# Performance work log

Measured on AMD Instinct MI355X. Metric: run time of the kernel, lower is better.

## Reference

```python
import jax, jax.numpy as jnp
import numpy as np

N_NODES = 50000
IN_CH, HID, OUT_CH = 512, 128, 64
N_EDGES = 800000


def gcn_conv(x, edge_index, W, b, num_nodes):
    # PyG GCNConv: add self-loops, symmetric deg^{-1/2} normalization,
    # linear transform then scatter-add aggregation at target nodes.
    row, col = edge_index[0], edge_index[1]
    loop = jnp.arange(num_nodes, dtype=row.dtype)
    rows = jnp.concatenate([row, loop])  # sources
    cols = jnp.concatenate([col, loop])  # targets
    deg = jax.ops.segment_sum(jnp.ones_like(cols, dtype=x.dtype), cols, num_segments=num_nodes)
    dinv = jnp.where(deg > 0, jax.lax.rsqrt(deg), 0.0)
    norm = dinv[rows] * dinv[cols]  # [E+N]
    h = x @ W  # [N, out]
    msg = norm[:, None] * h[rows]  # gather + scale
    out = jax.ops.segment_sum(msg, cols, num_segments=num_nodes)
    return out + b


def setup_inputs() -> dict:
    key = jax.random.key(0)
    k = jax.random.split(key, 8)
    x = jax.random.normal(k[0], (N_NODES, IN_CH), dtype=jnp.float32)
    pos_edge_index = jax.random.randint(k[1], (2, N_EDGES), 0, N_NODES, dtype=jnp.int64 if jax.config.jax_enable_x64 else jnp.int32)
    neg_edge_index = jax.random.randint(k[2], (2, N_EDGES), 0, N_NODES, dtype=pos_edge_index.dtype)
    # Glorot-ish init for weights, zeros for bias (PyG default)
    W1 = jax.random.normal(k[3], (IN_CH, HID), dtype=jnp.float32) * (1.0 / np.sqrt(IN_CH))
    b1 = jnp.zeros((HID,), dtype=jnp.float32)
    W2 = jax.random.normal(k[4], (HID, OUT_CH), dtype=jnp.float32) * (1.0 / np.sqrt(HID))
    b2 = jnp.zeros((OUT_CH,), dtype=jnp.float32)
    return {"x": x, "pos_edge_index": pos_edge_index, "neg_edge_index": neg_edge_index,
            "W1": W1, "b1": b1, "W2": W2, "b2": b2}


def reference(x, pos_edge_index, neg_edge_index, W1, b1, W2, b2):
    n = x.shape[0]
    h = gcn_conv(x, pos_edge_index, W1, b1, n)
    h = jax.nn.relu(h)
    z = gcn_conv(h, pos_edge_index, W2, b2, n)  # encode
    edge_index = jnp.concatenate([pos_edge_index, neg_edge_index], axis=-1)
    # decode: per-edge dot product of endpoint embeddings
    logits = jnp.sum(z[edge_index[0]] * z[edge_index[1]], axis=-1)
    return logits
```

## Files before the change

kernel.cpp:

```cpp
#include <hip/hip_runtime.h>

#define WAVE 64
#define CAP 64

typedef __bf16 v8bf __attribute__((ext_vector_type(8)));
typedef __bf16 v4bf __attribute__((ext_vector_type(4)));
typedef __bf16 v2bf __attribute__((ext_vector_type(2)));
typedef float f32x4 __attribute__((ext_vector_type(4)));

__device__ __forceinline__ void async16(void* lds, const void* g) {
    __builtin_amdgcn_global_load_lds((const __attribute__((address_space(1))) void*)g,
                                     (__attribute__((address_space(3))) void*)lds, 16, 0, 0);
}

__global__ __launch_bounds__(256) void prep_kernel(const float* __restrict__ W1,
                                                   const float* __restrict__ W2,
                                                   __bf16* __restrict__ Wt1hi,
                                                   __bf16* __restrict__ Wt1lo,
                                                   __bf16* __restrict__ Wt2hi,
                                                   __bf16* __restrict__ Wt2lo) {
    int b = blockIdx.x;
    int tid = threadIdx.x;
    if (b < 256) {
        int idx = b * 256 + tid;
        int k = idx >> 7, n = idx & 127;
        float v = W1[idx];
        __bf16 h = (__bf16)v;
        Wt1hi[n * 512 + k] = h;
        Wt1lo[n * 512 + k] = (__bf16)(v - (float)h);
    } else {
        int idx = (b - 256) * 256 + tid;
        int k = idx >> 6, n = idx & 63;
        float v = W2[idx];
        __bf16 h = (__bf16)v;
        Wt2hi[n * 128 + k] = h;
        Wt2lo[n * 128 + k] = (__bf16)(v - (float)h);
    }
}

template <int NC, int KK, bool OBF16, bool FILL>
__global__ __launch_bounds__(256, 2) void gemm_fill_kernel(
    const float* __restrict__ A, const __bf16* __restrict__ Bhi,
    const __bf16* __restrict__ Blo, void* __restrict__ Cout, int M, int NG,
    const int* __restrict__ ei, int E, int* __restrict__ cursor,
    int* __restrict__ srcs) {
    constexpr int BK = 32;
    constexpr int NT = NC / 16;
    constexpr int NIT = KK / BK;
    constexpr int CHB = NC / 16;

    __shared__ float sA[2][128 * 32];
    __shared__ __bf16 sB[2][2][NC * 32];

    const int tid = threadIdx.x;

    if (FILL && blockIdx.x >= NG) {
        int bb = (blockIdx.x - NG) * 512;
#pragma unroll
        for (int j = 0; j < 2; ++j) {
            int e = bb + tid + j * 256;
            if (e < E) {
                int dst = ei[E + e];
                int p = atomicAdd(&cursor[dst], 1);
                if (p < CAP) srcs[(size_t)dst * CAP + p] = ei[e];
            }
        }
        return;
    }

    const int lane = tid & 63;
    const int wv = tid >> 6;
    const int ln15 = lane & 15;
    const int quad = lane >> 4;
    const int rowBase = blockIdx.x * 128;

    auto stageA = [&](int buf, int k0) {
#pragma unroll
        for (int i = 0; i < 4; ++i) {
            int c = wv + i * 4;
            int row = c * 8 + (lane >> 3);
            int p = lane & 7;
            int grow = rowBase + row;
            if (grow > M - 1) grow = M - 1;
            int gcol = k0 + ((p ^ (row & 7)) << 2);
            async16(&sA[buf][c * 256], A + (size_t)grow * KK + gcol);
        }
    };
    auto stageB = [&](int buf, int k0) {
        for (int i = wv; i < CHB; i += 4) {
            int row = i * 16 + (lane >> 2);
            int p = lane & 3;
            int gk = k0 + ((p ^ ((row >> 1) & 3)) << 3);
            async16(&sB[buf][0][i * 512], Bhi + (size_t)row * KK + gk);
            async16(&sB[buf][1][i * 512], Blo + (size_t)row * KK + gk);
        }
    };

    f32x4 acc[2][NT];
#pragma unroll
    for (int rt = 0; rt < 2; ++rt)
#pragma unroll
        for (int t = 0; t < NT; ++t) acc[rt][t] = (f32x4){0.f, 0.f, 0.f, 0.f};

    stageA(0, 0);
    stageB(0, 0);
    __syncthreads();

    int cur = 0;
    for (int it = 0; it < NIT; ++it) {
        if (it + 1 < NIT) {
            stageA(cur ^ 1, (it + 1) * BK);
            stageB(cur ^ 1, (it + 1) * BK);
        }

        v8bf ah[2], al[2];
#pragma unroll
        for (int rt = 0; rt < 2; ++rt) {
            int row = wv * 32 + rt * 16 + ln15;
            int sw = row & 7;
            const float* base = &sA[cur][row * 32];
            f32x4 u = *(const f32x4*)(base + (((2 * quad) ^ sw) << 2));
            f32x4 v = *(const f32x4*)(base + (((2 * quad + 1) ^ sw) << 2));
            float f[8] = {u.x, u.y, u.z, u.w, v.x, v.y, v.z, v.w};
#pragma unroll
            for (int j = 0; j < 8; ++j) {
                __bf16 h = (__bf16)f[j];
                ah[rt][j] = h;
                al[rt][j] = (__bf16)(f[j] - (float)h);
            }
        }

#pragma unroll
        for (int t = 0; t < NT; ++t) {
            int row = t * 16 + ln15;
            int sw = (row >> 1) & 3;
            v8bf bh = *(const v8bf*)&sB[cur][0][row * 32 + ((quad ^ sw) << 3)];
            v8bf bl = *(const v8bf*)&sB[cur][1][row * 32 + ((quad ^ sw) << 3)];
#pragma unroll
            for (int rt = 0; rt < 2; ++rt) {
                acc[rt][t] = __builtin_amdgcn_mfma_f32_16x16x32_bf16(ah[rt], bh, acc[rt][t], 0, 0, 0);
                acc[rt][t] = __builtin_amdgcn_mfma_f32_16x16x32_bf16(al[rt], bh, acc[rt][t], 0, 0, 0);
                acc[rt][t] = __builtin_amdgcn_mfma_f32_16x16x32_bf16(ah[rt], bl, acc[rt][t], 0, 0, 0);
            }
        }

        __syncthreads();
        cur ^= 1;
    }

#pragma unroll
    for (int rt = 0; rt < 2; ++rt) {
#pragma unroll
        for (int r = 0; r < 4; ++r) {
            int grow = rowBase + wv * 32 + rt * 16 + quad * 4 + r;
            if (grow < M) {
#pragma unroll
                for (int t = 0; t < NT; ++t) {
                    float v = acc[rt][t][r];
                    if (OBF16)
                        ((__bf16*)Cout)[(size_t)grow * NC + t * 16 + ln15] = (__bf16)v;
                    else
                        ((float*)Cout)[(size_t)grow * NC + t * 16 + ln15] = v;
                }
            }
        }
    }
}

template <int F, bool RELU, bool BF16OUT>
__global__ __launch_bounds__(256) void gather_agg_bf16(const __bf16* __restrict__ hs,
                                                       const int* __restrict__ counts,
                                                       const int* __restrict__ srcs,
                                                       const float* __restrict__ bias,
                                                       void* __restrict__ outp, int N) {
    int node = blockIdx.x * 4 + (int)(threadIdx.x >> 6);
    if (node >= N) return;
    int lane = threadIdx.x & 63;
    int cnt = counts[node];
    if (cnt > CAP) cnt = CAP;
    int beg = node * CAP;
    int end = beg + cnt;
    float dn = rsqrtf((float)cnt + 1.0f);

    if constexpr (F == 128) {
        int col = 2 * lane;
        float a0, a1;
        {
            v2bf s = *(const v2bf*)&hs[(size_t)node * F + col];
            a0 = dn * (float)s[0];
            a1 = dn * (float)s[1];
        }
        int e = beg;
        for (; e + 4 <= end; e += 4) {
            int s0 = srcs[e], s1 = srcs[e + 1], s2 = srcs[e + 2], s3 = srcs[e + 3];
            float d0 = rsqrtf((float)counts[s0] + 1.0f);
            float d1 = rsqrtf((float)counts[s1] + 1.0f);
            float d2 = rsqrtf((float)counts[s2] + 1.0f);
            float d3 = rsqrtf((float)counts[s3] + 1.0f);
            v2bf r0 = *(const v2bf*)&hs[(size_t)s0 * F + col];
            v2bf r1 = *(const v2bf*)&hs[(size_t)s1 * F + col];
            v2bf r2 = *(const v2bf*)&hs[(size_t)s2 * F + col];
            v2bf r3 = *(const v2bf*)&hs[(size_t)s3 * F + col];
            a0 += d0 * (float)r0[0] + d1 * (float)r1[0] + d2 * (float)r2[0] + d3 * (float)r3[0];
            a1 += d0 * (float)r0[1] + d1 * (float)r1[1] + d2 * (float)r2[1] + d3 * (float)r3[1];
        }
        for (; e < end; ++e) {
            int s0 = srcs[e];
            float d0 = rsqrtf((float)counts[s0] + 1.0f);
            v2bf r0 = *(const v2bf*)&hs[(size_t)s0 * F + col];
            a0 += d0 * (float)r0[0];
            a1 += d0 * (float)r0[1];
        }
        float2 bv = *(const float2*)&bias[col];
        float v0 = dn * a0 + bv.x;
        float v1 = dn * a1 + bv.y;
        if (RELU) {
            v0 = fmaxf(v0, 0.f);
            v1 = fmaxf(v1, 0.f);
        }
        if (BF16OUT) {
            v2bf o;
            o[0] = (__bf16)v0;
            o[1] = (__bf16)v1;
            *(v2bf*)&((__bf16*)outp)[(size_t)node * F + col] = o;
        } else {
            *(float2*)&((float*)outp)[(size_t)node * F + col] = make_float2(v0, v1);
        }
    } else {
        int q = lane >> 4;
        int sl = lane & 15;
        int col = sl * 4;
        float a0 = 0.f, a1 = 0.f, a2 = 0.f, a3 = 0.f;
        if (q == 0) {
            v4bf s = *(const v4bf*)&hs[(size_t)node * F + col];
            a0 = dn * (float)s[0]; a1 = dn * (float)s[1];
            a2 = dn * (float)s[2]; a3 = dn * (float)s[3];
        }
        int e = beg + q;
        for (; e + 4 < end; e += 8) {
            int s0 = srcs[e], s1 = srcs[e + 4];
            float d0 = rsqrtf((float)counts[s0] + 1.0f);
            float d1 = rsqrtf((float)counts[s1] + 1.0f);
            v4bf r0 = *(const v4bf*)&hs[(size_t)s0 * F + col];
            v4bf r1 = *(const v4bf*)&hs[(size_t)s1 * F + col];
            a0 += d0 * (float)r0[0] + d1 * (float)r1[0];
            a1 += d0 * (float)r0[1] + d1 * (float)r1[1];
            a2 += d0 * (float)r0[2] + d1 * (float)r1[2];
            a3 += d0 * (float)r0[3] + d1 * (float)r1[3];
        }
        if (e < end) {
            int s0 = srcs[e];
            float d0 = rsqrtf((float)counts[s0] + 1.0f);
            v4bf r0 = *(const v4bf*)&hs[(size_t)s0 * F + col];
            a0 += d0 * (float)r0[0]; a1 += d0 * (float)r0[1];
            a2 += d0 * (float)r0[2]; a3 += d0 * (float)r0[3];
        }
        a0 += __shfl_xor(a0, 16); a0 += __shfl_xor(a0, 32);
        a1 += __shfl_xor(a1, 16); a1 += __shfl_xor(a1, 32);
        a2 += __shfl_xor(a2, 16); a2 += __shfl_xor(a2, 32);
        a3 += __shfl_xor(a3, 16); a3 += __shfl_xor(a3, 32);
        if (q == 0) {
            float4 bv = *(const float4*)&bias[col];
            float v0 = dn * a0 + bv.x;
            float v1 = dn * a1 + bv.y;
            float v2 = dn * a2 + bv.z;
            float v3 = dn * a3 + bv.w;
            if (RELU) {
                v0 = fmaxf(v0, 0.f); v1 = fmaxf(v1, 0.f);
                v2 = fmaxf(v2, 0.f); v3 = fmaxf(v3, 0.f);
            }
            if (BF16OUT) {
                v4bf o;
                o[0] = (__bf16)v0; o[1] = (__bf16)v1;
                o[2] = (__bf16)v2; o[3] = (__bf16)v3;
                *(v4bf*)&((__bf16*)outp)[(size_t)node * F + col] = o;
            } else {
                *(float4*)&((float*)outp)[(size_t)node * F + col] =
                    make_float4(v0, v1, v2, v3);
            }
        }
    }
}

__global__ __launch_bounds__(256) void decode_bf16_kernel(const __bf16* __restrict__ z,
                                                          const int* __restrict__ pos,
                                                          const int* __restrict__ neg, int E,
                                                          float* __restrict__ out) {
    int tid = blockIdx.x * blockDim.x + threadIdx.x;
    int g = tid >> 2;
    int l = tid & 3;
    int total = 2 * E;
    if (g >= total) return;
    int src, dst;
    if (g < E) {
        src = pos[g];
        dst = pos[E + g];
    } else {
        int e = g - E;
        src = neg[e];
        dst = neg[E + e];
    }
    const __bf16* zs = z + (size_t)src * 64 + l * 16;
    const __bf16* zd = z + (size_t)dst * 64 + l * 16;
    v8bf a0 = *(const v8bf*)zs;
    v8bf a1 = *(const v8bf*)(zs + 8);
    v8bf b0 = *(const v8bf*)zd;
    v8bf b1 = *(const v8bf*)(zd + 8);
    float p = 0.f;
#pragma unroll
    for (int j = 0; j < 8; ++j) p += (float)a0[j] * (float)b0[j] + (float)a1[j] * (float)b1[j];
    p += __shfl_xor(p, 1);
    p += __shfl_xor(p, 2);
    if (l == 0) out[g] = p;
}

extern "C" void kernel_launch(void* const* d_in, const int* in_sizes, int n_in, void* d_out,
                              int out_size, void* d_ws, size_t ws_size, hipStream_t stream) {
    const float* x = (const float*)d_in[0];
    const int* pos_ei = (const int*)d_in[1];
    const int* neg_ei = (const int*)d_in[2];
    const float* W1 = (const float*)d_in[3];
    const float* b1 = (const float*)d_in[4];
    const float* W2 = (const float*)d_in[5];
    const float* b2 = (const float*)d_in[6];
    float* out = (float*)d_out;

    const int IN = 512, HID = 128, OUT = 64;
    const int N = in_sizes[0] / IN;
    const int E = in_sizes[1] / 2;

    size_t nAlign = ((size_t)N + 255) & ~(size_t)255;
    float* p = (float*)d_ws;
    float* h1 = p; p += (size_t)N * HID;
    __bf16* hs1 = (__bf16*)p; p += (size_t)N * HID / 2;
    __bf16* hs2 = (__bf16*)p; p += (size_t)N * OUT / 2;
    __bf16* zbf = (__bf16*)p; p += (size_t)N * OUT / 2;
    int* cursor = (int*)p; p += nAlign;
    int* srcs = (int*)p; p += (size_t)N * CAP;
    __bf16* Wt1hi = (__bf16*)p; p += (size_t)IN * HID / 2;
    __bf16* Wt1lo = (__bf16*)p; p += (size_t)IN * HID / 2;
    __bf16* Wt2hi = (__bf16*)p; p += (size_t)HID * OUT / 2;
    __bf16* Wt2lo = (__bf16*)p; p += (size_t)HID * OUT / 2;

    const int NG = (N + 127) / 128;
    const int NF = (E + 511) / 512;

    hipMemsetAsync(cursor, 0, (size_t)N * sizeof(int), stream);
    prep_kernel<<<288, 256, 0, stream>>>(W1, W2, Wt1hi, Wt1lo, Wt2hi, Wt2lo);

    gemm_fill_kernel<128, 512, true, true><<<NG + NF, 256, 0, stream>>>(
        x, Wt1hi, Wt1lo, hs1, N, NG, pos_ei, E, cursor, srcs);
    gather_agg_bf16<128, true, false>
        <<<(N + 3) / 4, 256, 0, stream>>>(hs1, cursor, srcs, b1, h1, N);

    gemm_fill_kernel<64, 128, true, false><<<NG, 256, 0, stream>>>(
        h1, Wt2hi, Wt2lo, hs2, N, NG, nullptr, 0, nullptr, nullptr);
    gather_agg_bf16<64, false, true>
        <<<(N + 3) / 4, 256, 0, stream>>>(hs2, cursor, srcs, b2, zbf, N);

    decode_bf16_kernel<<<((size_t)2 * E * 4 + 255) / 256, 256, 0, stream>>>(
        zbf, pos_ei, neg_ei, E, out);
}
```

Baseline: 325.0 us.

## Drop LDS staging in GEMM; load A and pre-tiled B directly into registers

The GEMM no longer uses double-buffered shared memory or barriers. Each lane loads its A fragment straight from global memory into registers with one-step register prefetch. B is read directly from a weight layout that the prep kernel now writes pre-tiled as [k/32][n][32]. Removing LDS allows the occupancy hint to rise to 3 blocks per SM. The trade-off is that B fragments are now re-read from global/L2 by every wave instead of shared through LDS, and memory latency is hidden by only a single prefetch.

Result: slower. 337.7 us (+3.9%).

```diff
diff --git a/kernel.cpp b/kernel.cpp
--- a/kernel.cpp
+++ b/kernel.cpp
@@ -7,11 +7,6 @@
 typedef __bf16 v4bf __attribute__((ext_vector_type(4)));
 typedef __bf16 v2bf __attribute__((ext_vector_type(2)));
 typedef float f32x4 __attribute__((ext_vector_type(4)));
-
-__device__ __forceinline__ void async16(void* lds, const void* g) {
-    __builtin_amdgcn_global_load_lds((const __attribute__((address_space(1))) void*)g,
-                                     (__attribute__((address_space(3))) void*)lds, 16, 0, 0);
-}
 
 __global__ __launch_bounds__(256) void prep_kernel(const float* __restrict__ W1,
                                                    const float* __restrict__ W2,
@@ -26,31 +21,28 @@
         int k = idx >> 7, n = idx & 127;
         float v = W1[idx];
         __bf16 h = (__bf16)v;
-        Wt1hi[n * 512 + k] = h;
-        Wt1lo[n * 512 + k] = (__bf16)(v - (float)h);
+        int o = (k >> 5) * (128 * 32) + n * 32 + (k & 31);
+        Wt1hi[o] = h;
+        Wt1lo[o] = (__bf16)(v - (float)h);
     } else {
         int idx = (b - 256) * 256 + tid;
         int k = idx >> 6, n = idx & 63;
         float v = W2[idx];
         __bf16 h = (__bf16)v;
-        Wt2hi[n * 128 + k] = h;
-        Wt2lo[n * 128 + k] = (__bf16)(v - (float)h);
+        int o = (k >> 5) * (64 * 32) + n * 32 + (k & 31);
+        Wt2hi[o] = h;
+        Wt2lo[o] = (__bf16)(v - (float)h);
     }
 }
 
 template <int NC, int KK, bool OBF16, bool FILL>
-__global__ __launch_bounds__(256, 2) void gemm_fill_kernel(
+__global__ __launch_bounds__(256, 3) void gemm_fill_kernel(
     const float* __restrict__ A, const __bf16* __restrict__ Bhi,
     const __bf16* __restrict__ Blo, void* __restrict__ Cout, int M, int NG,
     const int* __restrict__ ei, int E, int* __restrict__ cursor,
     int* __restrict__ srcs) {
-    constexpr int BK = 32;
     constexpr int NT = NC / 16;
-    constexpr int NIT = KK / BK;
-    constexpr int CHB = NC / 16;
-
-    __shared__ float sA[2][128 * 32];
-    __shared__ __bf16 sB[2][2][NC * 32];
+    constexpr int NK = KK / 32;
 
     const int tid = threadIdx.x;
 
@@ -74,78 +66,64 @@
     const int quad = lane >> 4;
     const int rowBase = blockIdx.x * 128;
 
-    auto stageA = [&](int buf, int k0) {
-#pragma unroll
-        for (int i = 0; i < 4; ++i) {
-            int c = wv + i * 4;
-            int row = c * 8 + (lane >> 3);
-            int p = lane & 7;
-            int grow = rowBase + row;
-            if (grow > M - 1) grow = M - 1;
-            int gcol = k0 + ((p ^ (row & 7)) << 2);
-            async16(&sA[buf][c * 256], A + (size_t)grow * KK + gcol);
+    int r0 = rowBase + wv * 32 + ln15;
+    int r1 = r0 + 16;
+    if (r0 > M - 1) r0 = M - 1;
+    if (r1 > M - 1) r1 = M - 1;
+    const float* aP0 = A + (size_t)r0 * KK + quad * 8;
+    const float* aP1 = A + (size_t)r1 * KK + quad * 8;
+    const __bf16* bhP = Bhi + ln15 * 32 + quad * 8 + 2048;
+    const __bf16* blP = Blo + ln15 * 32 + quad * 8 + 2048;
+
+    f32x4 acc[2][NT];
+#pragma unroll
+    for (int rt = 0; rt < 2; ++rt)
+#pragma unroll
+        for (int t = 0; t < NT; ++t) acc[rt][t] = (f32x4){0.f, 0.f, 0.f, 0.f};
+
+    float4 aR[4];
+    aR[0] = *(const float4*)(aP0);
+    aR[1] = *(const float4*)(aP0 + 4);
+    aR[2] = *(const float4*)(aP1);
+    aR[3] = *(const float4*)(aP1 + 4);
+
+    auto cvt8 = [&](const float4& u, const float4& v, v8bf& h, v8bf& l) {
+        float f[8] = {u.x, u.y, u.z, u.w, v.x, v.y, v.z, v.w};
+#pragma unroll
+        for (int j = 0; j < 8; ++j) {
+            __bf16 hh = (__bf16)f[j];
+            h[j] = hh;
+            l[j] = (__bf16)(f[j] - (float)hh);
         }
     };
-    auto stageB = [&](int buf, int k0) {
-        for (int i = wv; i < CHB; i += 4) {
-            int row = i * 16 + (lane >> 2);
-            int p = lane & 3;
-            int gk = k0 + ((p ^ ((row >> 1) & 3)) << 3);
-            async16(&sB[buf][0][i * 512], Bhi + (size_t)row * KK + gk);
-            async16(&sB[buf][1][i * 512], Blo + (size_t)row * KK + gk);
-        }
-    };
-
-    f32x4 acc[2][NT];
-#pragma unroll
-    for (int rt = 0; rt < 2; ++rt)
-#pragma unroll
-        for (int t = 0; t < NT; ++t) acc[rt][t] = (f32x4){0.f, 0.f, 0.f, 0.f};
-
-    stageA(0, 0);
-    stageB(0, 0);
-    __syncthreads();
-
-    int cur = 0;
-    for (int it = 0; it < NIT; ++it) {
-        if (it + 1 < NIT) {
-            stageA(cur ^ 1, (it + 1) * BK);
-            stageB(cur ^ 1, (it + 1) * BK);
-        }
-
+
+    for (int ks = 0; ks < NK; ++ks) {
         v8bf ah[2], al[2];
-#pragma unroll
-        for (int rt = 0; rt < 2; ++rt) {
-            int row = wv * 32 + rt * 16 + ln15;
-            int sw = row & 7;
-            const float* base = &sA[cur][row * 32];
-            f32x4 u = *(const f32x4*)(base + (((2 * quad) ^ sw) << 2));
-            f32x4 v = *(const f32x4*)(base + (((2 * quad + 1) ^ sw) << 2));
-            float f[8] = {u.x, u.y, u.z, u.w, v.x, v.y, v.z, v.w};
-#pragma unroll
-            for (int j = 0; j < 8; ++j) {
-                __bf16 h = (__bf16)f[j];
-                ah[rt][j] = h;
-                al[rt][j] = (__bf16)(f[j] - (float)h);
-            }
+        cvt8(aR[0], aR[1], ah[0], al[0]);
+        cvt8(aR[2], aR[3], ah[1], al[1]);
+
+        if (ks + 1 < NK) {
+            aP0 += 32;
+            aP1 += 32;
+            aR[0] = *(const float4*)(aP0);
+            aR[1] = *(const float4*)(aP0 + 4);
+            aR[2] = *(const float4*)(aP1);
+            aR[3] = *(const float4*)(aP1 + 4);
         }
 
 #pragma unroll
         for (int t = 0; t < NT; ++t) {
-            int row = t * 16 + ln15;
-            int sw = (row >> 1) & 3;
-            v8bf bh = *(const v8bf*)&sB[cur][0][row * 32 + ((quad ^ sw) << 3)];
-            v8bf bl = *(const v8bf*)&sB[cur][1][row * 32 + ((quad ^ sw) << 3)];
-#pragma unroll
-            for (int rt = 0; rt < 2; ++rt) {
-                acc[rt][t] = __builtin_amdgcn_mfma_f32_16x16x32_bf16(ah[rt], bh, acc[rt][t], 0, 0, 0);
-                acc[rt][t] = __builtin_amdgcn_mfma_f32_16x16x32_bf16(al[rt], bh, acc[rt][t], 0, 0, 0);
-                acc[rt][t] = __builtin_amdgcn_mfma_f32_16x16x32_bf16(ah[rt], bl, acc[rt][t], 0, 0, 0);
-            }
-        }
-
-        __syncthreads();
-        cur ^= 1;
+            v8bf bh = *(const v8bf*)(bhP + t * 512 - 2048);
+            v8bf bl = *(const v8bf*)(blP + t * 512 - 2048);
+            acc[0][t] = __builtin_amdgcn_mfma_f32_16x16x32_bf16(ah[0], bh, acc[0][t], 0, 0, 0);
+            acc[0][t] = __builtin_amdgcn_mfma_f32_16x16x32_bf16(al[0], bh, acc[0][t], 0, 0, 0);
+            acc[0][t] = __builtin_amdgcn_mfma_f32_16x16x32_bf16(ah[0], bl, acc[0][t], 0, 0, 0);
+            acc[1][t] = __builtin_amdgcn_mfma_f32_16x16x32_bf16(ah[1], bh, acc[1][t], 0, 0, 0);
+            acc[1][t] = __builtin_amdgcn_mfma_f32_16x16x32_bf16(al[1], bh, acc[1][t], 0, 0, 0);
+            acc[1][t] = __builtin_amdgcn_mfma_f32_16x16x32_bf16(ah[1], bl, acc[1][t], 0, 0, 0);
+        }
+        bhP += NC * 32;
+        blP += NC * 32;
     }
 
 #pragma unroll
```
